# Performance work log

Hardware: AMD Instinct MI355X
Metric: run time of the kernel (lower is better)

The kernel has to match this reference:

```python
import jax, jax.numpy as jnp
import numpy as np

B, S, D = 2, 2048, 1024
H, DH = 16, 64
DM = 4096
NEG = 1e10


def setup_inputs() -> dict:
    key = jax.random.key(0)
    ks = jax.random.split(key, 8)
    sc = 1.0 / np.sqrt(D)
    return {
        "x": jax.random.normal(ks[0], (B, S, D), jnp.float32),
        "W_Q": jax.random.normal(ks[1], (H, DH, D), jnp.float32) * sc,
        "W_K": jax.random.normal(ks[2], (H, DH, D), jnp.float32) * sc,
        "W_V": jax.random.normal(ks[3], (H, DH, D), jnp.float32) * sc,
        "W_O": jax.random.normal(ks[4], (D, H * DH), jnp.float32) * sc,
        "W_in": jax.random.normal(ks[5], (DM, D), jnp.float32) * sc,
        "b_in": jnp.zeros((DM,), jnp.float32),
        "W_out": jax.random.normal(ks[6], (D, DM), jnp.float32) * sc,
        "b_out": jnp.zeros((D,), jnp.float32),
    }


def reference(x, W_Q, W_K, W_V, W_O, W_in, b_in, W_out, b_out):
    b, s, d = x.shape
    d_head = W_Q.shape[1]
    # --- Attention (faithful to original einsum/mask formulation) ---
    q = jnp.einsum('ihd,bpd->biph', W_Q, x)
    k = jnp.einsum('ihd,bpd->biph', W_K, x)
    v = jnp.einsum('ihd,bpd->biph', W_V, x)
    scores = jnp.einsum('biph,biqh->biqp', k, q)  # [b,i,q,p]
    # original: t.tril(scores) - 1e10 * (1 - triu(ones)) ; mask buffer is triu
    triu = jnp.triu(jnp.ones((s, s), x.dtype))
    masked = jnp.tril(scores) - NEG * (1.0 - triu)
    attn = jax.nn.softmax(masked / np.sqrt(d_head), axis=-1)
    z = jnp.einsum('biph,biqp->biqh', v, attn)          # [b,i,q,h]
    z_flat = z.transpose(0, 2, 1, 3).reshape(b, s, -1)   # b q (i h)
    attn_out = jnp.einsum('df,bqf->bqd', W_O, z_flat)
    # --- Block residual structure (as written: x = attn(x); x = x + x) ---
    mid = attn_out + attn_out
    # --- MLP ---
    pre = jnp.einsum('md,bpd->bpm', W_in, mid) + b_in
    h = jax.nn.relu(pre)
    mlp_out = jnp.einsum('dm,bpm->bpd', W_out, h) + b_out
    return mid + mlp_out
```

## Files before the change

kernel.cpp:

```cpp
#include <hip/hip_runtime.h>
#include <hip/hip_bf16.h>
#include <stdint.h>

typedef unsigned short ushort_t;
typedef __attribute__((ext_vector_type(8))) short short8;
typedef __attribute__((ext_vector_type(4))) float floatx4;

#define DEV __device__ __forceinline__

DEV ushort_t f2b(float f) {
  uint32_t x = __float_as_uint(f);
  uint32_t r = (x + 0x7FFFu + ((x >> 16) & 1u)) >> 16;
  return (ushort_t)r;
}
DEV float b2f(ushort_t u) { return __uint_as_float(((uint32_t)u) << 16); }

DEV void async16(const ushort_t* g, ushort_t* l) {
  __builtin_amdgcn_global_load_lds(
      (const __attribute__((address_space(1))) void*)g,
      (__attribute__((address_space(3))) void*)l, 16, 0, 0);
}

struct Cvt7 {
  const float* src[7];
  ushort_t* dst[7];
  float scale[7];
  unsigned start[8];
};
__global__ void cvt_all(Cvt7 a) {
  unsigned idx = blockIdx.x * blockDim.x + threadIdx.x;
  if (idx >= a.start[7]) return;
  int seg = 0;
#pragma unroll
  for (int j = 1; j < 7; j++) seg += (idx >= a.start[j]) ? 1 : 0;
  unsigned off = idx - a.start[seg];
  float sc = a.scale[seg];
  float4 v = ((const float4*)a.src[seg])[off];
  ((ushort4*)a.dst[seg])[off] =
      make_ushort4(f2b(v.x * sc), f2b(v.y * sc), f2b(v.z * sc), f2b(v.w * sc));
}

template <int MODE, int MT, int SWZ>
__launch_bounds__(256)
__global__ void gemm_bt(const ushort_t* __restrict__ A, const ushort_t* __restrict__ Bm,
                        int M, int N, int Kd, int ldk,
                        ushort_t* __restrict__ outB, float* __restrict__ outF,
                        const float* __restrict__ bias) {
  constexpr int TM = 32 * MT;
  __shared__ alignas(16) ushort_t As[TM * 64];
  __shared__ alignas(16) ushort_t Bs[128 * 64];
  const int tid = threadIdx.x;
  const int wave = tid >> 6, lane = tid & 63;
  const int wm = wave >> 1, wn = wave & 1;

  int bx, by;
  if constexpr (SWZ == 1) {
    const int f = blockIdx.x + gridDim.x * blockIdx.y;
    by = (f & 7) + 8 * (f / (8 * gridDim.x));
    bx = (f >> 3) % gridDim.x;
  } else if constexpr (SWZ == 2) {
    const int x = blockIdx.x, y = blockIdx.y;
    bx = 2 * (x & 3) + (y & 1);
    by = (y >> 1) + 32 * (x >> 2);
  } else {
    bx = blockIdx.x; by = blockIdx.y;
  }
  const int m0 = by * TM, n0 = bx * 128;
  const int kz = blockIdx.z * Kd;

  floatx4 acc[MT][4];
#pragma unroll
  for (int i = 0; i < MT; i++)
#pragma unroll
    for (int j = 0; j < 4; j++) acc[i][j] = (floatx4){0.f, 0.f, 0.f, 0.f};

  const int r8 = lane >> 3;
  const int scol = (((lane & 7) ^ (r8 & 7)) * 8);
  const ushort_t* gA = A + (size_t)(m0 + wave * (TM / 4) + r8) * ldk + kz + scol;
  const ushort_t* gB = Bm + (size_t)(n0 + wave * 32 + r8) * ldk + kz + scol;
  ushort_t* lA = As + wave * (TM / 4) * 64;
  ushort_t* lB = Bs + wave * 2048;

  const int fr = lane & 15, fq = lane >> 4;
  const int sw = fr & 7;
  const ushort_t* rdA = As + (wm * 16 * MT + fr) * 64;
  const ushort_t* rdB = Bs + (wn * 64 + fr) * 64;

  for (int k0 = 0; k0 < Kd; k0 += 64) {
#pragma unroll
    for (int j = 0; j < MT; j++) async16(gA + (size_t)j * 8 * ldk, lA + j * 512);
#pragma unroll
    for (int j = 0; j < 4; j++) async16(gB + (size_t)j * 8 * ldk, lB + j * 512);
    gA += 64; gB += 64;
    __syncthreads();
#pragma unroll
    for (int h = 0; h < 2; h++) {
      const int co = ((h * 4 + fq) ^ sw) * 8;
      short8 af[MT], bfv[4];
#pragma unroll
      for (int mt = 0; mt < MT; mt++) af[mt] = *(const short8*)(rdA + mt * 16 * 64 + co);
#pragma unroll
      for (int nt = 0; nt < 4; nt++) bfv[nt] = *(const short8*)(rdB + nt * 16 * 64 + co);
#pragma unroll
      for (int mt = 0; mt < MT; mt++)
#pragma unroll
        for (int nt = 0; nt < 4; nt++)
          acc[mt][nt] = __builtin_amdgcn_mfma_f32_16x16x32_bf16(af[mt], bfv[nt], acc[mt][nt], 0, 0, 0);
    }
    __syncthreads();
  }

  const int crow = m0 + wm * 16 * MT + (lane >> 4) * 4;
  const int ccol = n0 + wn * 64 + (lane & 15);
  const size_t zoff = (size_t)blockIdx.z * M * N;
#pragma unroll
  for (int mt = 0; mt < MT; mt++)
#pragma unroll
    for (int nt = 0; nt < 4; nt++) {
      floatx4 a = acc[mt][nt];
#pragma unroll
      for (int r = 0; r < 4; r++) {
        const int gm = crow + mt * 16 + r;
        const int gn = ccol + nt * 16;
        const size_t idx = (size_t)gm * N + gn;
        float v = a[r];
        if constexpr (MODE == 0) {
          outB[idx] = f2b(v);
        } else if constexpr (MODE == 1) {
          outB[idx] = f2b(v);
          outF[idx] = v + bias[gn];
        } else if constexpr (MODE == 2) {
          float t = v + bias[gn];
          outB[idx] = f2b(t > 0.f ? t : 0.f);
        } else {
          outF[zoff + idx] = v;
        }
      }
    }
}

template <int MODE>
__launch_bounds__(512, 2)
__global__ void gemm256(const ushort_t* __restrict__ A, const ushort_t* __restrict__ Bm,
                        int M, int N, int Kd, int ldk,
                        ushort_t* __restrict__ outB, float* __restrict__ outF,
                        const float* __restrict__ bias) {
  __shared__ alignas(16) ushort_t As[4][256 * 32];
  __shared__ alignas(16) ushort_t Bs[4][256 * 32];
  const int tid = threadIdx.x;
  const int lane = tid & 63;
  const int wave = tid >> 6;
  const int wm = wave >> 2, wn = wave & 3;

  const int gy = gridDim.y;
  int f = blockIdx.x + gridDim.x * blockIdx.y;
  {
    const int nwg = gridDim.x * gy;
    const int q = nwg >> 3, rr = nwg & 7;
    const int xcd = f & 7, ix = f >> 3;
    f = (xcd < rr ? xcd * (q + 1) : rr * (q + 1) + (xcd - rr) * q) + ix;
  }
  const int bx = f / gy, by = f - gy * bx;
  const int m0 = by * 256, n0 = bx * 256;
  const size_t kz = (size_t)blockIdx.z * Kd;

  floatx4 acc[8][4];
#pragma unroll
  for (int i = 0; i < 8; i++)
#pragma unroll
    for (int j = 0; j < 4; j++) acc[i][j] = (floatx4){0.f, 0.f, 0.f, 0.f};

  const int rloc = tid >> 2, cch = tid & 3;
  const int gcol = ((cch ^ ((rloc >> 1) & 3)) * 8);
  const ushort_t* gA = A + (size_t)(m0 + rloc) * ldk + kz + gcol;
  const ushort_t* gB = Bm + (size_t)(n0 + rloc) * ldk + kz + gcol;
  const int lofs = rloc * 32 + cch * 8;

#define STGA32(bufi, kofs)                                              \
  {                                                                     \
    async16(gA + (kofs), &As[bufi][lofs]);                              \
    async16(gA + (size_t)128 * ldk + (kofs), &As[bufi][4096 + lofs]);   \
  }
#define STGB32(bufi, kofs)                                              \
  {                                                                     \
    async16(gB + (kofs), &Bs[bufi][lofs]);                              \
    async16(gB + (size_t)128 * ldk + (kofs), &Bs[bufi][4096 + lofs]);   \
  }

  const int NT = Kd >> 5;
  STGA32(0, 0) STGB32(0, 0)
  if (NT > 1) { STGA32(1, 32) STGB32(1, 32) }
  if (NT > 2) { STGA32(2, 64) STGB32(2, 64) }
  if (NT > 2) asm volatile("s_waitcnt vmcnt(8)" ::: "memory");
  else if (NT > 1) asm volatile("s_waitcnt vmcnt(4)" ::: "memory");
  else asm volatile("s_waitcnt vmcnt(0)" ::: "memory");
  __builtin_amdgcn_s_barrier();

  const int fr = lane & 15, fq = lane >> 4;
  const int co = ((fq ^ ((fr >> 1) & 3)) * 8);
  const int aoff = (wm * 128 + fr) * 32 + co;
  const int boff = (wn * 64 + fr) * 32 + co;

  for (int kt = 0; kt < NT; ++kt) {
    const int cb = kt & 3;
    const int pb = (kt + 3) & 3;
    const int kof = (kt + 3) * 32;
    const bool sp = (kt + 3) < NT;
    const ushort_t* Ab = As[cb];
    const ushort_t* Bb = Bs[cb];
    short8 av[4], bv[4];

#pragma unroll
    for (int i = 0; i < 4; i++) av[i] = *(const short8*)(Ab + aoff + i * 512);
#pragma unroll
    for (int j = 0; j < 4; j++) bv[j] = *(const short8*)(Bb + boff + j * 512);
    if (sp) STGA32(pb, kof)
    __builtin_amdgcn_s_barrier();
    asm volatile("s_waitcnt lgkmcnt(0)" ::: "memory");
    __builtin_amdgcn_s_setprio(1);
#pragma unroll
    for (int i = 0; i < 4; i++)
#pragma unroll
      for (int j = 0; j < 4; j++)
        acc[i][j] = __builtin_amdgcn_mfma_f32_16x16x32_bf16(av[i], bv[j], acc[i][j], 0, 0, 0);
    __builtin_amdgcn_s_setprio(0);
    __builtin_amdgcn_s_barrier();

#pragma unroll
    for (int i = 0; i < 4; i++) av[i] = *(const short8*)(Ab + aoff + 2048 + i * 512);
    if (sp) STGB32(pb, kof)
    __builtin_amdgcn_s_barrier();
    asm volatile("s_waitcnt lgkmcnt(0)" ::: "memory");
    __builtin_amdgcn_s_setprio(1);
#pragma unroll
    for (int i = 0; i < 4; i++)
#pragma unroll
      for (int j = 0; j < 4; j++)
        acc[4 + i][j] = __builtin_amdgcn_mfma_f32_16x16x32_bf16(av[i], bv[j], acc[4 + i][j], 0, 0, 0);
    __builtin_amdgcn_s_setprio(0);
    if (kt + 3 < NT) asm volatile("s_waitcnt vmcnt(8)" ::: "memory");
    else if (kt + 2 < NT) asm volatile("s_waitcnt vmcnt(4)" ::: "memory");
    else asm volatile("s_waitcnt vmcnt(0)" ::: "memory");
    __builtin_amdgcn_s_barrier();
  }
#undef STGA32
#undef STGB32

  const int crow = m0 + wm * 128 + (lane >> 4) * 4;
  const int ccol = n0 + wn * 64 + (lane & 15);
#pragma unroll
  for (int mt = 0; mt < 8; mt++)
#pragma unroll
    for (int nt = 0; nt < 4; nt++) {
      floatx4 a = acc[mt][nt];
#pragma unroll
      for (int r = 0; r < 4; r++) {
        const int gm = crow + mt * 16 + r;
        const int gn = ccol + nt * 16;
        const size_t idx = (size_t)gm * N + gn;
        if constexpr (MODE == 0) {
          outB[idx] = f2b(a[r]);
        } else if constexpr (MODE == 2) {
          float t = a[r] + bias[gn];
          outB[idx] = f2b(t > 0.f ? t : 0.f);
        } else {
          outF[idx] = a[r];
        }
      }
    }
}

__launch_bounds__(256)
__global__ void reduce2(const float4* __restrict__ P, float4* __restrict__ out, int n4) {
  int i = blockIdx.x * blockDim.x + threadIdx.x;
  int st = gridDim.x * blockDim.x;
  for (; i < n4; i += st) {
    float4 a = out[i];
    float4 p0 = P[i], p1 = P[i + 1048576];
    a.x += p0.x + p1.x;
    a.y += p0.y + p1.y;
    a.z += p0.z + p1.z;
    a.w += p0.w + p1.w;
    out[i] = a;
  }
}

__launch_bounds__(256)
__global__ void attn1(const ushort_t* __restrict__ qkv,
                      float* __restrict__ eG, float* __restrict__ psumG) {
  const int c = blockIdx.x & 63;
  const int i = (blockIdx.x >> 6) & 15;
  const int b = blockIdx.x >> 10;
  const int t = threadIdx.x, wave = t >> 6, h = t & 63;
  const size_t rowbase = (size_t)b * 2048 * 3072;
  float vacc = 0.f;
#pragma unroll
  for (int r = 0; r < 8; r++) {
    const int s = c * 32 + wave * 8 + r;
    const size_t rb = rowbase + (size_t)s * 3072 + i * 64 + h;
    float q = b2f(qkv[rb]);
    float k = b2f(qkv[rb + 1024]);
    float v = b2f(qkv[rb + 2048]);
    float d = q * k;
#pragma unroll
    for (int off = 32; off > 0; off >>= 1) d += __shfl_xor(d, off, 64);
    if (h == 0) eG[((size_t)(b * 16 + i)) * 2048 + s] = __expf(d * 0.125f);
    vacc += v;
  }
  __shared__ float vs[4][64];
  vs[wave][h] = vacc;
  __syncthreads();
  if (t < 64)
    psumG[(((size_t)(b * 16 + i)) * 64 + c) * 64 + t] =
        vs[0][t] + vs[1][t] + vs[2][t] + vs[3][t];
}

__launch_bounds__(256)
__global__ void attn2(const ushort_t* __restrict__ qkv,
                      const float* __restrict__ eG, const float* __restrict__ psumG,
                      ushort_t* __restrict__ Z) {
  const int wave = threadIdx.x >> 6, h = threadIdx.x & 63;
  const int c = (blockIdx.x & 15) * 4 + wave;
  const int i = (blockIdx.x >> 4) & 15;
  const int b = blockIdx.x >> 8;
  const size_t rowbase = (size_t)b * 2048 * 3072;
  const size_t pbase = ((size_t)(b * 16 + i)) * 64;
  float r0 = 0.f, r1 = 0.f, r2 = 0.f, r3 = 0.f;
  {
    int cc = c + 1;
    for (; cc + 3 < 64; cc += 4) {
      r0 += psumG[(pbase + cc) * 64 + h];
      r1 += psumG[(pbase + cc + 1) * 64 + h];
      r2 += psumG[(pbase + cc + 2) * 64 + h];
      r3 += psumG[(pbase + cc + 3) * 64 + h];
    }
    for (; cc < 64; cc++) r0 += psumG[(pbase + cc) * 64 + h];
  }
  float run = (r0 + r1) + (r2 + r3);
  const size_t ebase = ((size_t)(b * 16 + i)) * 2048;
  for (int t4 = 1; t4 >= 0; t4--) {
    float vv[16], num[16], rcp[16];
#pragma unroll
    for (int j = 0; j < 16; j++) {
      const int s = c * 32 + t4 * 16 + j;
      vv[j] = b2f(qkv[rowbase + (size_t)s * 3072 + 2048 + i * 64 + h]);
      float e = eG[ebase + s];
      num[j] = e * vv[j];
      float d = e + (float)(2047 - s);
      float r = __builtin_amdgcn_rcpf(d);
      rcp[j] = r * (2.f - d * r);
    }
#pragma unroll
    for (int j = 15; j >= 0; j--) {
      const int s = c * 32 + t4 * 16 + j;
      float z = (num[j] + run) * rcp[j];
      Z[((size_t)b * 2048 + s) * 1024 + i * 64 + h] = f2b(z);
      run += vv[j];
    }
  }
}

extern "C" void kernel_launch(void* const* d_in, const int* in_sizes, int n_in,
                              void* d_out, int out_size, void* d_ws, size_t ws_size,
                              hipStream_t stream) {
  const float* x     = (const float*)d_in[0];
  const float* W_Q   = (const float*)d_in[1];
  const float* W_K   = (const float*)d_in[2];
  const float* W_V   = (const float*)d_in[3];
  const float* W_O   = (const float*)d_in[4];
  const float* W_in  = (const float*)d_in[5];
  const float* b_in  = (const float*)d_in[6];
  const float* W_out = (const float*)d_in[7];
  const float* b_out = (const float*)d_in[8];
  float* out = (float*)d_out;

  char* base = (char*)d_ws;
  const size_t MB = 1048576;
  ushort_t* Xb    = (ushort_t*)(base + 0 * MB);
  ushort_t* Wqkv  = (ushort_t*)(base + 8 * MB);
  ushort_t* WOb   = (ushort_t*)(base + 14 * MB);
  ushort_t* Z     = (ushort_t*)(base + 16 * MB);
  ushort_t* QKV   = (ushort_t*)(base + 24 * MB);
  ushort_t* midb  = (ushort_t*)(base + 48 * MB);
  ushort_t* Winb  = (ushort_t*)(base + 56 * MB);
  ushort_t* Woutb = (ushort_t*)(base + 64 * MB);
  ushort_t* Hb    = (ushort_t*)(base + 72 * MB);
  float*    P     = (float*)(base + 0 * MB);
  float*    psumG = (float*)(base + 72 * MB);
  float*    eG    = (float*)(base + 72 * MB + 524288);

  Cvt7 ca;
  ca.src[0] = x;     ca.dst[0] = Xb;               ca.scale[0] = 1.f;
  ca.src[1] = W_Q;   ca.dst[1] = Wqkv;             ca.scale[1] = 1.f;
  ca.src[2] = W_K;   ca.dst[2] = Wqkv + 1048576;   ca.scale[2] = 1.f;
  ca.src[3] = W_V;   ca.dst[3] = Wqkv + 2097152;   ca.scale[3] = 1.f;
  ca.src[4] = W_O;   ca.dst[4] = WOb;              ca.scale[4] = 2.f;
  ca.src[5] = W_in;  ca.dst[5] = Winb;             ca.scale[5] = 1.f;
  ca.src[6] = W_out; ca.dst[6] = Woutb;            ca.scale[6] = 1.f;
  unsigned n4s[7] = {1048576, 262144, 262144, 262144, 262144, 1048576, 1048576};
  unsigned acc4 = 0;
  for (int j = 0; j < 7; j++) { ca.start[j] = acc4; acc4 += n4s[j]; }
  ca.start[7] = acc4;
  cvt_all<<<dim3((acc4 + 255) / 256), dim3(256), 0, stream>>>(ca);

  gemm_bt<0, 4, 0><<<dim3(24, 32), 256, 0, stream>>>(Xb, Wqkv, 4096, 3072, 1024, 1024,
                                                     QKV, nullptr, nullptr);
  attn1<<<dim3(2048), 256, 0, stream>>>(QKV, eG, psumG);
  attn2<<<dim3(512), 256, 0, stream>>>(QKV, eG, psumG, Z);
  gemm_bt<1, 2, 1><<<dim3(8, 64), 256, 0, stream>>>(Z, WOb, 4096, 1024, 1024, 1024,
                                                    midb, out, b_out);
  gemm256<2><<<dim3(16, 16), 512, 0, stream>>>(midb, Winb, 4096, 4096, 1024, 1024,
                                               Hb, nullptr, b_in);
  gemm_bt<3, 2, 2><<<dim3(8, 64, 2), 256, 0, stream>>>(Hb, Woutb, 4096, 1024, 2048, 4096,
                                                       nullptr, P, nullptr);
  reduce2<<<dim3(1024), 256, 0, stream>>>((const float4*)P, (float4*)out, 1048576);
}
```

Baseline: 281.6 us.

## Shrink MLP-in GEMM tile to 128x256 with double buffering and higher occupancy

Replaces the 256x256-tile, four-stage LDS pipeline GEMM used for the MLP up-projection with a 128x256-tile variant. It double-buffers LDS and raises the occupancy hint so several workgroups can share a CU. The grid doubles to 512 workgroups, so latency is meant to be hidden by running more workgroups at once rather than by prefetching deeper. In exchange, each workgroup reuses less data per tile, and every iteration waits for all outstanding global loads (vmcnt(0)), which can expose memory latency.

After: 453.3 us. 1.61x slower.

```diff
diff --git a/kernel.cpp b/kernel.cpp
--- a/kernel.cpp
+++ b/kernel.cpp
@@ -140,13 +140,13 @@
 }
 
 template <int MODE>
-__launch_bounds__(512, 2)
-__global__ void gemm256(const ushort_t* __restrict__ A, const ushort_t* __restrict__ Bm,
+__launch_bounds__(512, 6)
+__global__ void gemm128(const ushort_t* __restrict__ A, const ushort_t* __restrict__ Bm,
                         int M, int N, int Kd, int ldk,
                         ushort_t* __restrict__ outB, float* __restrict__ outF,
                         const float* __restrict__ bias) {
-  __shared__ alignas(16) ushort_t As[4][256 * 32];
-  __shared__ alignas(16) ushort_t Bs[4][256 * 32];
+  __shared__ alignas(16) ushort_t As[2][128 * 32];
+  __shared__ alignas(16) ushort_t Bs[2][256 * 32];
   const int tid = threadIdx.x;
   const int lane = tid & 63;
   const int wave = tid >> 6;
@@ -161,95 +161,83 @@
     f = (xcd < rr ? xcd * (q + 1) : rr * (q + 1) + (xcd - rr) * q) + ix;
   }
   const int bx = f / gy, by = f - gy * bx;
-  const int m0 = by * 256, n0 = bx * 256;
-  const size_t kz = (size_t)blockIdx.z * Kd;
-
-  floatx4 acc[8][4];
-#pragma unroll
-  for (int i = 0; i < 8; i++)
+  const int m0 = by * 128, n0 = bx * 256;
+
+  floatx4 acc[4][4];
+#pragma unroll
+  for (int i = 0; i < 4; i++)
 #pragma unroll
     for (int j = 0; j < 4; j++) acc[i][j] = (floatx4){0.f, 0.f, 0.f, 0.f};
 
   const int rloc = tid >> 2, cch = tid & 3;
   const int gcol = ((cch ^ ((rloc >> 1) & 3)) * 8);
-  const ushort_t* gA = A + (size_t)(m0 + rloc) * ldk + kz + gcol;
-  const ushort_t* gB = Bm + (size_t)(n0 + rloc) * ldk + kz + gcol;
+  const ushort_t* gA = A + (size_t)(m0 + rloc) * ldk + gcol;
+  const ushort_t* gB = Bm + (size_t)(n0 + rloc) * ldk + gcol;
   const int lofs = rloc * 32 + cch * 8;
 
-#define STGA32(bufi, kofs)                                              \
+#define STA128(d, kof) { async16(gA + (kof), &As[d][lofs]); }
+#define STB256(d, kof)                                                  \
   {                                                                     \
-    async16(gA + (kofs), &As[bufi][lofs]);                              \
-    async16(gA + (size_t)128 * ldk + (kofs), &As[bufi][4096 + lofs]);   \
-  }
-#define STGB32(bufi, kofs)                                              \
-  {                                                                     \
-    async16(gB + (kofs), &Bs[bufi][lofs]);                              \
-    async16(gB + (size_t)128 * ldk + (kofs), &Bs[bufi][4096 + lofs]);   \
+    async16(gB + (kof), &Bs[d][lofs]);                                  \
+    async16(gB + (size_t)128 * ldk + (kof), &Bs[d][4096 + lofs]);       \
   }
 
   const int NT = Kd >> 5;
-  STGA32(0, 0) STGB32(0, 0)
-  if (NT > 1) { STGA32(1, 32) STGB32(1, 32) }
-  if (NT > 2) { STGA32(2, 64) STGB32(2, 64) }
-  if (NT > 2) asm volatile("s_waitcnt vmcnt(8)" ::: "memory");
-  else if (NT > 1) asm volatile("s_waitcnt vmcnt(4)" ::: "memory");
-  else asm volatile("s_waitcnt vmcnt(0)" ::: "memory");
+  STA128(0, 0) STB256(0, 0)
+  asm volatile("s_waitcnt vmcnt(0)" ::: "memory");
   __builtin_amdgcn_s_barrier();
 
   const int fr = lane & 15, fq = lane >> 4;
   const int co = ((fq ^ ((fr >> 1) & 3)) * 8);
-  const int aoff = (wm * 128 + fr) * 32 + co;
+  const int aoff = (wm * 64 + fr) * 32 + co;
   const int boff = (wn * 64 + fr) * 32 + co;
 
-  for (int kt = 0; kt < NT; ++kt) {
-    const int cb = kt & 3;
-    const int pb = (kt + 3) & 3;
-    const int kof = (kt + 3) * 32;
-    const bool sp = (kt + 3) < NT;
-    const ushort_t* Ab = As[cb];
-    const ushort_t* Bb = Bs[cb];
+  for (int t = 0; t < NT; ++t) {
+    const int d = t & 1, o = d ^ 1;
+    const int kof = (t + 1) << 5;
+    const bool st = (t + 1) < NT;
+    const ushort_t* Ah = &As[d][0];
+    const ushort_t* Bh = &Bs[d][0];
     short8 av[4], bv[4];
 
 #pragma unroll
-    for (int i = 0; i < 4; i++) av[i] = *(const short8*)(Ab + aoff + i * 512);
-#pragma unroll
-    for (int j = 0; j < 4; j++) bv[j] = *(const short8*)(Bb + boff + j * 512);
-    if (sp) STGA32(pb, kof)
+    for (int mi = 0; mi < 4; mi++) av[mi] = *(const short8*)(Ah + aoff + mi * 512);
+#pragma unroll
+    for (int ni = 0; ni < 2; ni++) bv[ni] = *(const short8*)(Bh + boff + ni * 512);
+    if (st) STA128(o, kof)
     __builtin_amdgcn_s_barrier();
     asm volatile("s_waitcnt lgkmcnt(0)" ::: "memory");
     __builtin_amdgcn_s_setprio(1);
 #pragma unroll
-    for (int i = 0; i < 4; i++)
-#pragma unroll
-      for (int j = 0; j < 4; j++)
-        acc[i][j] = __builtin_amdgcn_mfma_f32_16x16x32_bf16(av[i], bv[j], acc[i][j], 0, 0, 0);
+    for (int mi = 0; mi < 4; mi++)
+#pragma unroll
+      for (int ni = 0; ni < 2; ni++)
+        acc[mi][ni] = __builtin_amdgcn_mfma_f32_16x16x32_bf16(av[mi], bv[ni], acc[mi][ni], 0, 0, 0);
     __builtin_amdgcn_s_setprio(0);
     __builtin_amdgcn_s_barrier();
 
 #pragma unroll
-    for (int i = 0; i < 4; i++) av[i] = *(const short8*)(Ab + aoff + 2048 + i * 512);
-    if (sp) STGB32(pb, kof)
+    for (int ni = 0; ni < 2; ni++) bv[2 + ni] = *(const short8*)(Bh + boff + (ni + 2) * 512);
+    if (st) STB256(o, kof)
     __builtin_amdgcn_s_barrier();
     asm volatile("s_waitcnt lgkmcnt(0)" ::: "memory");
     __builtin_amdgcn_s_setprio(1);
 #pragma unroll
-    for (int i = 0; i < 4; i++)
-#pragma unroll
-      for (int j = 0; j < 4; j++)
-        acc[4 + i][j] = __builtin_amdgcn_mfma_f32_16x16x32_bf16(av[i], bv[j], acc[4 + i][j], 0, 0, 0);
+    for (int mi = 0; mi < 4; mi++)
+#pragma unroll
+      for (int ni = 0; ni < 2; ni++)
+        acc[mi][ni + 2] = __builtin_amdgcn_mfma_f32_16x16x32_bf16(av[mi], bv[2 + ni], acc[mi][ni + 2], 0, 0, 0);
     __builtin_amdgcn_s_setprio(0);
-    if (kt + 3 < NT) asm volatile("s_waitcnt vmcnt(8)" ::: "memory");
-    else if (kt + 2 < NT) asm volatile("s_waitcnt vmcnt(4)" ::: "memory");
-    else asm volatile("s_waitcnt vmcnt(0)" ::: "memory");
+    if (st) asm volatile("s_waitcnt vmcnt(0)" ::: "memory");
     __builtin_amdgcn_s_barrier();
   }
-#undef STGA32
-#undef STGB32
-
-  const int crow = m0 + wm * 128 + (lane >> 4) * 4;
+#undef STA128
+#undef STB256
+
+  const int crow = m0 + wm * 64 + (lane >> 4) * 4;
   const int ccol = n0 + wn * 64 + (lane & 15);
 #pragma unroll
-  for (int mt = 0; mt < 8; mt++)
+  for (int mt = 0; mt < 4; mt++)
 #pragma unroll
     for (int nt = 0; nt < 4; nt++) {
       floatx4 a = acc[mt][nt];
@@ -261,8 +249,8 @@
         if constexpr (MODE == 0) {
           outB[idx] = f2b(a[r]);
         } else if constexpr (MODE == 2) {
-          float t = a[r] + bias[gn];
-          outB[idx] = f2b(t > 0.f ? t : 0.f);
+          float t2 = a[r] + bias[gn];
+          outB[idx] = f2b(t2 > 0.f ? t2 : 0.f);
         } else {
           outF[idx] = a[r];
         }
@@ -409,7 +397,7 @@
   attn2<<<dim3(512), 256, 0, stream>>>(QKV, eG, psumG, Z);
   gemm_bt<1, 2, 1><<<dim3(8, 64), 256, 0, stream>>>(Z, WOb, 4096, 1024, 1024, 1024,
                                                     midb, out, b_out);
-  gemm256<2><<<dim3(16, 16), 512, 0, stream>>>(midb, Winb, 4096, 4096, 1024, 1024,
+  gemm128<2><<<dim3(16, 32), 512, 0, stream>>>(midb, Winb, 4096, 4096, 1024, 1024,
                                                Hb, nullptr, b_in);
   gemm_bt<3, 2, 2><<<dim3(8, 64, 2), 256, 0, stream>>>(Hb, Woutb, 4096, 1024, 2048, 4096,
                                                        nullptr, P, nullptr);
```
